# Optimization experiments

Measured on AMD Instinct MI355X. Metric: run time of the kernel, lower is better.

The kernel has to match this reference:

```python
import jax, jax.numpy as jnp
import numpy as np
from jax import lax

B, S, T = 32, 100, 4
NUM_C2, NUM_C3, NUM_D, DV = 500, 2000, 1000, 128


def setup_inputs():
    key = jax.random.key(0)
    ks = jax.random.split(key, 25)
    s = 0.05
    def nrm(k, shape):
        return jax.random.normal(k, shape, dtype=jnp.float32) * s
    return {
        "c2_seq": jax.random.randint(ks[0], (B, S), 0, NUM_C2),
        "c3_seq": jax.random.randint(ks[1], (B, S, T), 1, NUM_C3 + 1),  # 0 is padding; use all-valid tags
        "d_seq": jax.random.randint(ks[2], (B, S), 0, NUM_D),
        "r_seq": jax.random.randint(ks[3], (B, S), 0, 2),
        "D_emb": nrm(ks[4], (NUM_D, 1)),
        "R_emb": nrm(ks[5], (2, DV)),
        "v_c2": nrm(ks[6], (DV,)),
        "v_c3": nrm(ks[7], (DV,)),
        "v_d": nrm(ks[8], (DV,)),
        "W_ih": nrm(ks[9], (3 * DV, 2 * DV)),
        "W_hh": nrm(ks[10], (3 * DV, DV)),
        "b_ih": nrm(ks[11], (3 * DV,)),
        "b_hh": nrm(ks[12], (3 * DV,)),
        "l1_W1": nrm(ks[13], (DV, DV)), "l1_b1": nrm(ks[14], (DV,)),
        "l1_W2": nrm(ks[15], (1, DV)), "l1_b2": nrm(ks[16], (1,)),
        "l2_W1": nrm(ks[17], (DV, 4 * DV)), "l2_b1": nrm(ks[18], (DV,)),
        "l2_W2": nrm(ks[19], (1, DV)), "l2_b2": nrm(ks[20], (1,)),
        "l3_W1": nrm(ks[21], (DV, 4 * DV)), "l3_b1": nrm(ks[22], (DV,)),
        "l3_W2": nrm(ks[23], (1, DV)), "l3_b2": nrm(ks[24], (1,)),
    }


def _mlp(x, W1, b1, W2, b2):
    # Linear -> ReLU -> (Dropout: identity in eval) -> Linear -> (Dropout)
    return jnp.maximum(x @ W1.T + b1, 0.0) @ W2.T + b2


def _gru(x_seq, h0, W_ih, W_hh, b_ih, b_hh):
    # torch.nn.GRU math, batch_first
    def step(h, x):
        gi = x @ W_ih.T + b_ih
        gh = h @ W_hh.T + b_hh
        i_r, i_z, i_n = jnp.split(gi, 3, axis=-1)
        h_r, h_z, h_n = jnp.split(gh, 3, axis=-1)
        r = jax.nn.sigmoid(i_r + h_r)
        z = jax.nn.sigmoid(i_z + h_z)
        n = jnp.tanh(i_n + r * h_n)
        h_new = (1.0 - z) * n + z * h
        return h_new, h_new
    _, hs = lax.scan(step, h0, jnp.swapaxes(x_seq, 0, 1))
    return jnp.swapaxes(hs, 0, 1)


def _forward(c2_seq, c3_seq, d_seq, r_seq, p):
    (D_emb, R_emb, v_c2, v_c3, v_d, W_ih, W_hh, b_ih, b_hh,
     l1_W1, l1_b1, l1_W2, l1_b2, l2_W1, l2_b1, l2_W2, l2_b2,
     l3_W1, l3_b1, l3_W2, l3_b2) = p
    Bn = c2_seq.shape[0]
    gamma = D_emb[d_seq]                      # [B,S,1]
    v_d_seq = gamma * v_d                     # [B,S,DV]
    v_r_seq = R_emb[r_seq]                    # [B,S,DV]
    h0 = jnp.zeros((Bn, DV), dtype=v_d_seq.dtype)
    h_seq = _gru(jnp.concatenate([v_d_seq, v_r_seq], -1), h0, W_ih, W_hh, b_ih, b_hh)
    alpha_seq = _mlp(h_seq, l1_W1, l1_b1, l1_W2, l1_b2)[..., 0]   # [B,S]

    def step(carry, xs):
        C2, C3 = carry
        c2, c3, vd, vr = xs                                      # [B],[B,T],[B,DV],[B,DV]
        mask = (c3 != 0).astype(C3.dtype)                        # [B,T]
        w = mask / mask.sum(-1, keepdims=True)
        beta2 = jnp.take_along_axis(C2, c2[:, None], axis=-1)    # [B,1]
        beta3 = jnp.take_along_axis(C3, c3, axis=-1)             # [B,T]
        beta3_bar = (beta3 * w).sum(-1)                          # [B]
        vc2 = beta2 * v_c2                                       # [B,DV]
        vc3 = beta3[..., None] * v_c3                            # [B,T,DV]
        vc3_bar = beta3_bar[:, None] * v_c3                      # [B,DV]
        new_c2 = _mlp(jnp.concatenate([vc2, vc3_bar, vd, vr], -1),
                      l2_W1, l2_b1, l2_W2, l2_b2)[:, 0]          # [B]
        feat3 = jnp.concatenate([
            jnp.broadcast_to(vc2[:, None, :], vc3.shape), vc3,
            jnp.broadcast_to(vd[:, None, :], vc3.shape),
            jnp.broadcast_to(vr[:, None, :], vc3.shape)], -1)    # [B,T,4*DV]
        new_c3 = _mlp(feat3, l3_W1, l3_b1, l3_W2, l3_b2)[..., 0]  # [B,T]
        oh2 = jax.nn.one_hot(c2, NUM_C2, dtype=C2.dtype)          # [B,NC2]
        oh3 = jax.nn.one_hot(c3, NUM_C3 + 1, dtype=C3.dtype) * mask[..., None]  # [B,T,NC3+1]
        multi = oh3.sum(1)
        C2n = C2 * (1.0 - oh2) + new_c2[:, None] * oh2
        C3n = C3 * (1.0 - multi) + (new_c3[..., None] * oh3).sum(1)
        return (C2n, C3n), (C2n, C3n)

    C2_0 = jnp.zeros((Bn, NUM_C2), dtype=jnp.float32)
    C3_0 = jnp.zeros((Bn, NUM_C3 + 1), dtype=jnp.float32)
    xs = (jnp.swapaxes(c2_seq, 0, 1), jnp.swapaxes(c3_seq, 0, 1),
          jnp.swapaxes(v_d_seq, 0, 1), jnp.swapaxes(v_r_seq, 0, 1))
    _, (C2_seq, C3_seq) = lax.scan(step, (C2_0, C3_0), xs)
    C2_seq = jnp.swapaxes(C2_seq, 0, 1)   # [B,S,NUM_C2]
    C3_seq = jnp.swapaxes(C3_seq, 0, 1)   # [B,S,NUM_C3+1]
    return alpha_seq, h_seq, C2_seq, C3_seq


def reference(c2_seq, c3_seq, d_seq, r_seq, D_emb, R_emb, v_c2, v_c3, v_d,
              W_ih, W_hh, b_ih, b_hh, l1_W1, l1_b1, l1_W2, l1_b2,
              l2_W1, l2_b1, l2_W2, l2_b2, l3_W1, l3_b1, l3_W2, l3_b2):
    p = (D_emb, R_emb, v_c2, v_c3, v_d, W_ih, W_hh, b_ih, b_hh,
         l1_W1, l1_b1, l1_W2, l1_b2, l2_W1, l2_b1, l2_W2, l2_b2,
         l3_W1, l3_b1, l3_W2, l3_b2)
    return _forward(c2_seq, c3_seq, d_seq, r_seq, p)
```

## Files before the change

### kernel.cpp

```cpp
#include <hip/hip_runtime.h>

#define BB   32
#define SS   100
#define TT   4
#define NCC2 500
#define NC3P 2001
#define DD   128

#define LDSF 14680

typedef _Float16 half2v __attribute__((ext_vector_type(2)));

#if defined(__has_builtin)
#if __has_builtin(__builtin_amdgcn_fdot2)
#define HAVE_FDOT2 1
#endif
#endif

__device__ __forceinline__ float fast_rcp(float x) { return __builtin_amdgcn_rcpf(x); }

__device__ __forceinline__ float dpp_sum64(float x) {
    x += __int_as_float(__builtin_amdgcn_update_dpp(0, __float_as_int(x), 0x111, 0xf, 0xf, true));
    x += __int_as_float(__builtin_amdgcn_update_dpp(0, __float_as_int(x), 0x112, 0xf, 0xf, true));
    x += __int_as_float(__builtin_amdgcn_update_dpp(0, __float_as_int(x), 0x114, 0xf, 0xf, true));
    x += __int_as_float(__builtin_amdgcn_update_dpp(0, __float_as_int(x), 0x118, 0xf, 0xf, true));
    x += __int_as_float(__builtin_amdgcn_update_dpp(0, __float_as_int(x), 0x142, 0xa, 0xf, true));
    x += __int_as_float(__builtin_amdgcn_update_dpp(0, __float_as_int(x), 0x143, 0xc, 0xf, true));
    return x;
}

__device__ __forceinline__ float dpp_sum16(float x) {
    x += __int_as_float(__builtin_amdgcn_update_dpp(0, __float_as_int(x), 0x111, 0xf, 0xf, true));
    x += __int_as_float(__builtin_amdgcn_update_dpp(0, __float_as_int(x), 0x112, 0xf, 0xf, true));
    x += __int_as_float(__builtin_amdgcn_update_dpp(0, __float_as_int(x), 0x114, 0xf, 0xf, true));
    x += __int_as_float(__builtin_amdgcn_update_dpp(0, __float_as_int(x), 0x118, 0xf, 0xf, true));
    return x;
}

__device__ __forceinline__ float dot4(float4 a, float4 b) {
    return fmaf(a.x, b.x, fmaf(a.y, b.y, fmaf(a.z, b.z, a.w * b.w)));
}

__device__ __forceinline__ unsigned pk16(float a, float b) {
    return __builtin_bit_cast(unsigned, __builtin_amdgcn_cvt_pkrtz(a, b));
}
__device__ __forceinline__ uint4 packf16(float4 A, float4 B) {
    uint4 u;
    u.x = pk16(A.x, A.y); u.y = pk16(A.z, A.w);
    u.z = pk16(B.x, B.y); u.w = pk16(B.z, B.w);
    return u;
}

__device__ __forceinline__ float dot2acc(unsigned w, unsigned h, float acc) {
#ifdef HAVE_FDOT2
    return __builtin_amdgcn_fdot2(__builtin_bit_cast(half2v, w),
                                  __builtin_bit_cast(half2v, h), acc, false);
#else
    half2v a = __builtin_bit_cast(half2v, w), b = __builtin_bit_cast(half2v, h);
    acc = fmaf((float)a.x, (float)b.x, acc);
    return fmaf((float)a.y, (float)b.y, acc);
#endif
}

__global__ __launch_bounds__(768, 1) void k_main(
    const int* __restrict__ c2_seq, const int* __restrict__ c3_seq,
    const int* __restrict__ d_seq,  const int* __restrict__ r_seq,
    const float* __restrict__ D_emb, const float* __restrict__ Remb,
    const float* __restrict__ v_c2, const float* __restrict__ v_c3,
    const float* __restrict__ v_d,
    const float* __restrict__ W_ih, const float* __restrict__ W_hh,
    const float* __restrict__ b_ih, const float* __restrict__ b_hh,
    const float* __restrict__ l2W1, const float* __restrict__ l2b1,
    const float* __restrict__ l2W2, const float* __restrict__ l2b2,
    const float* __restrict__ l3W1, const float* __restrict__ l3b1,
    const float* __restrict__ l3W2, const float* __restrict__ l3b2,
    float* __restrict__ h_out, float* __restrict__ C2o, float* __restrict__ C3o)
{
    __shared__ __align__(16) float sh[LDSF];
    int* shi = (int*)sh;
    const int blk = blockIdx.x;
    const int t = threadIdx.x;

    if (blk < BB) {
        const int b  = blk;
        const int w  = t >> 6, l = t & 63;
        const int p4 = w & 3;
        const int j2 = (w >> 2) * 64 + l;
        const int jA = j2, jB = j2 + 192;
        const int kb = p4 * 32;

        uint4 wa0, wa1, wa2, wa3, wb0, wb1, wb2, wb3;
        {
            const float4* ra = (const float4*)(W_hh + jA * DD + kb);
            const float4* rb = (const float4*)(W_hh + jB * DD + kb);
            wa0 = packf16(ra[0], ra[1]); wa1 = packf16(ra[2], ra[3]);
            wa2 = packf16(ra[4], ra[5]); wa3 = packf16(ra[6], ra[7]);
            wb0 = packf16(rb[0], rb[1]); wb1 = packf16(rb[2], rb[3]);
            wb2 = packf16(rb[4], rb[5]); wb3 = packf16(rb[6], rb[7]);
        }

        {
            const float4* vd4 = (const float4*)(v_d + kb);
            const float4* r04 = (const float4*)(Remb + kb);
            const float4* r14 = (const float4*)(Remb + 128 + kb);
#pragma unroll
            for (int rr2 = 0; rr2 < 2; ++rr2) {
                const int j = rr2 ? jB : jA;
                const float4* wx = (const float4*)(W_ih + j * 256 + kb);
                const float4* wr = (const float4*)(W_ih + j * 256 + 128 + kb);
                float pd = 0.f, pr0 = 0.f, pr1 = 0.f;
#pragma unroll
                for (int i = 0; i < 8; ++i) {
                    float4 a = wx[i], c = wr[i];
                    float4 vd = vd4[i], r0 = r04[i], r1 = r14[i];
                    pd  = fmaf(a.x, vd.x, fmaf(a.y, vd.y, fmaf(a.z, vd.z, fmaf(a.w, vd.w, pd))));
                    pr0 = fmaf(c.x, r0.x, fmaf(c.y, r0.y, fmaf(c.z, r0.z, fmaf(c.w, r0.w, pr0))));
                    pr1 = fmaf(c.x, r1.x, fmaf(c.y, r1.y, fmaf(c.z, r1.z, fmaf(c.w, r1.w, pr1))));
                }
                sh[1880 + p4 * 388 + j] = pd;
                sh[3432 + p4 * 388 + j] = pr0;
                sh[4984 + p4 * 388 + j] = pr1;
            }
        }
        if (t < SS) {
            sh[1680 + t]  = D_emb[d_seq[b * SS + t]];
            shi[1780 + t] = r_seq[b * SS + t];
        }
        if (t < 64) ((unsigned*)sh)[t] = 0u;
        __syncthreads();

        float gd_r=0,gd_z=0,gd_n=0, g0_r=0,g0_z=0,g0_n=0, g1_r=0,g1_z=0,g1_n=0;
        float bi_r=0,bi_z=0,bi_n=0, bh_r=0,bh_z=0,bh_n=0, h = 0.f;
        if (t < DD) {
#pragma unroll
            for (int p = 0; p < 4; ++p) {
                gd_r += sh[1880 + p * 388 + t];
                gd_z += sh[1880 + p * 388 + 128 + t];
                gd_n += sh[1880 + p * 388 + 256 + t];
                g0_r += sh[3432 + p * 388 + t];
                g0_z += sh[3432 + p * 388 + 128 + t];
                g0_n += sh[3432 + p * 388 + 256 + t];
                g1_r += sh[4984 + p * 388 + t];
                g1_z += sh[4984 + p * 388 + 128 + t];
                g1_n += sh[4984 + p * 388 + 256 + t];
            }
            bi_r = b_ih[t]; bi_z = b_ih[t+128]; bi_n = b_ih[t+256];
            bh_r = b_hh[t]; bh_z = b_hh[t+128]; bh_n = b_hh[t+256];
        }
        __syncthreads();

        for (int s = 0; s < SS; ++s) {
            float aA = 0.f, aB = 0.f;
            {
                const uint4* hb = ((const uint4*)sh) + p4 * 4;
                uint4 h0 = hb[0], h1 = hb[1], h2 = hb[2], h3 = hb[3];
                aA = dot2acc(wa0.x, h0.x, aA); aA = dot2acc(wa0.y, h0.y, aA);
                aA = dot2acc(wa0.z, h0.z, aA); aA = dot2acc(wa0.w, h0.w, aA);
                aA = dot2acc(wa1.x, h1.x, aA); aA = dot2acc(wa1.y, h1.y, aA);
                aA = dot2acc(wa1.z, h1.z, aA); aA = dot2acc(wa1.w, h1.w, aA);
                aA = dot2acc(wa2.x, h2.x, aA); aA = dot2acc(wa2.y, h2.y, aA);
                aA = dot2acc(wa2.z, h2.z, aA); aA = dot2acc(wa2.w, h2.w, aA);
                aA = dot2acc(wa3.x, h3.x, aA); aA = dot2acc(wa3.y, h3.y, aA);
                aA = dot2acc(wa3.z, h3.z, aA); aA = dot2acc(wa3.w, h3.w, aA);
                aB = dot2acc(wb0.x, h0.x, aB); aB = dot2acc(wb0.y, h0.y, aB);
                aB = dot2acc(wb0.z, h0.z, aB); aB = dot2acc(wb0.w, h0.w, aB);
                aB = dot2acc(wb1.x, h1.x, aB); aB = dot2acc(wb1.y, h1.y, aB);
                aB = dot2acc(wb1.z, h1.z, aB); aB = dot2acc(wb1.w, h1.w, aB);
                aB = dot2acc(wb2.x, h2.x, aB); aB = dot2acc(wb2.y, h2.y, aB);
                aB = dot2acc(wb2.z, h2.z, aB); aB = dot2acc(wb2.w, h2.w, aB);
                aB = dot2acc(wb3.x, h3.x, aB); aB = dot2acc(wb3.y, h3.y, aB);
                aB = dot2acc(wb3.z, h3.z, aB); aB = dot2acc(wb3.w, h3.w, aB);
            }
            sh[128 + p4 * 388 + jA] = aA;
            sh[128 + p4 * 388 + jB] = aB;
            __syncthreads();
            if (t < DD) {
                float ghr = bh_r, ghz = bh_z, ghn = bh_n;
#pragma unroll
                for (int p = 0; p < 4; ++p) {
                    ghr += sh[128 + p * 388 + t];
                    ghz += sh[128 + p * 388 + 128 + t];
                    ghn += sh[128 + p * 388 + 256 + t];
                }
                float gamma = sh[1680 + s]; int rr = shi[1780 + s];
                float gir = fmaf(gamma, gd_r, (rr ? g1_r : g0_r) + bi_r);
                float giz = fmaf(gamma, gd_z, (rr ? g1_z : g0_z) + bi_z);
                float gin = fmaf(gamma, gd_n, (rr ? g1_n : g0_n) + bi_n);
                float r = fast_rcp(1.f + __expf(-(gir + ghr)));
                float z = fast_rcp(1.f + __expf(-(giz + ghz)));
                float n = 1.f - 2.f * fast_rcp(__expf(2.f * fmaf(r, ghn, gin)) + 1.f);
                h = (1.f - z) * n + z * h;
                ((_Float16*)sh)[t] = (_Float16)h;
                sh[1880 + s * DD + t] = h;
            }
            __syncthreads();
        }

        {
            const float4* hs = (const float4*)(sh + 1880);
            float4* hd = (float4*)(h_out + (size_t)b * SS * DD);
            for (int i = t; i < SS * DD / 4; i += 768) hd[i] = hs[i];
        }
    } else {
        const int sb = blk - BB;
        const int b = sb >> 2;
        const int q = sb & 3;

        {
            const int g = (t & 63) >> 4, c8 = ((t & 63) & 15) * 8;
            const float* vsrc = (g == 0) ? v_c2 : (g == 1) ? v_c3 : (g == 2) ? v_d : Remb;
            const float4 va  = *(const float4*)(vsrc + c8);
            const float4 vb  = *(const float4*)(vsrc + c8 + 4);
            const float4 va1 = *(const float4*)(Remb + 128 + c8);
            const float4 vb1 = *(const float4*)(Remb + 132 + c8);
            for (int r = t >> 6; r < 256; r += 12) {
                const float* W = (r < 128) ? l2W1 : l3W1;
                float* U = sh + ((r < 128) ? 3264 : 3904);
                const int i = r & 127;
                const float* wr = W + i * 512 + g * 128 + c8;
                const float4 w0 = *(const float4*)(wr);
                const float4 w1 = *(const float4*)(wr + 4);
                float p  = dot4(w0, va)  + dot4(w1, vb);
                float p1 = dot4(w0, va1) + dot4(w1, vb1);
                p  = dpp_sum16(p);
                p1 = dpp_sum16(p1);
                if ((t & 15) == 15) {
                    U[g * 128 + i] = p;
                    if (g == 3) U[512 + i] = p1;
                }
            }
        }
        for (int k = t; k < NCC2 + NC3P; k += 768) sh[k] = 0.f;
        for (int k = t; k < SS; k += 768) {
            shi[2504 + k] = c2_seq[b * SS + k];
            sh[3004 + k]  = D_emb[d_seq[b * SS + k]];
            shi[3104 + k] = r_seq[b * SS + k];
        }
        for (int k = t; k < SS; k += 768)
            reinterpret_cast<int4*>(shi + 2604)[k] = reinterpret_cast<const int4*>(c3_seq + b * SS * TT)[k];
        __syncthreads();

        if (t < 64) {
            float* C2s = sh;
            float* C3s = sh + NCC2;
            const float* u2 = sh + 3264;
            const float* u3 = sh + 3904;
            const float u2a0 = u2[t],        u2a1 = u2[64 + t];
            const float u2b0 = u2[128 + t],  u2b1 = u2[192 + t];
            const float u2c0 = u2[256 + t],  u2c1 = u2[320 + t];
            const float u2d00 = u2[384 + t], u2d01 = u2[448 + t];
            const float u2d10 = u2[512 + t], u2d11 = u2[576 + t];
            const float u3a0 = u3[t],        u3a1 = u3[64 + t];
            const float u3b0 = u3[128 + t],  u3b1 = u3[192 + t];
            const float u3c0 = u3[256 + t],  u3c1 = u3[320 + t];
            const float u3d00 = u3[384 + t], u3d01 = u3[448 + t];
            const float u3d10 = u3[512 + t], u3d11 = u3[576 + t];
            const float b2_0 = l2b1[t], b2_1 = l2b1[64 + t];
            const float w2_0 = l2W2[t], w2_1 = l2W2[64 + t];
            const float b3_0 = l3b1[t], b3_1 = l3b1[64 + t];
            const float w3_0 = l3W2[t], w3_1 = l3W2[64 + t];
            const float c2bias = l2b2[0], c3bias = l3b2[0];

            int  nc2 = shi[2504];
            int4 nc3 = reinterpret_cast<const int4*>(shi + 2604)[0];
            float ngam = sh[3004];
            int   nrr  = shi[3104];

            for (int s = 0; s < SS; ++s) {
                const int c2i = nc2;
                const int i0 = nc3.x, i1 = nc3.y, i2 = nc3.z, i3 = nc3.w;
                const float gamma = ngam;
                const int rr = nrr;
                if (s + 1 < SS) {
                    nc2 = shi[2504 + s + 1];
                    nc3 = reinterpret_cast<const int4*>(shi + 2604)[s + 1];
                    ngam = sh[3004 + s + 1];
                    nrr  = shi[3104 + s + 1];
                }

                const float beta2 = C2s[c2i];
                const bool k0 = (i0 != 0), k1 = (i1 != 0), k2 = (i2 != 0), k3 = (i3 != 0);
                const float m0 = k0 ? 1.f : 0.f, m1 = k1 ? 1.f : 0.f;
                const float m2 = k2 ? 1.f : 0.f, m3 = k3 ? 1.f : 0.f;
                const float bt0 = C3s[i0], bt1 = C3s[i1], bt2 = C3s[i2], bt3 = C3s[i3];
                const float msum = m0 + m1 + m2 + m3;
                const float b3bar = (bt0 * m0 + bt1 * m1 + bt2 * m2 + bt3 * m3) * fast_rcp(msum);

                const float ud20 = rr ? u2d10 : u2d00, ud21 = rr ? u2d11 : u2d01;
                const float ud30 = rr ? u3d10 : u3d00, ud31 = rr ? u3d11 : u3d01;

                float h20 = fmaf(beta2, u2a0, fmaf(b3bar, u2b0, fmaf(gamma, u2c0, ud20 + b2_0)));
                float h21 = fmaf(beta2, u2a1, fmaf(b3bar, u2b1, fmaf(gamma, u2c1, ud21 + b2_1)));
                float newc2 = dpp_sum64(fmaf(fmaxf(h20, 0.f), w2_0, fmaxf(h21, 0.f) * w2_1)) + c2bias;

                const float base30 = fmaf(beta2, u3a0, fmaf(gamma, u3c0, ud30 + b3_0));
                const float base31 = fmaf(beta2, u3a1, fmaf(gamma, u3c1, ud31 + b3_1));
                float ha, hb, q0, q1, q2, q3;
                ha = fmaf(bt0, u3b0, base30); hb = fmaf(bt0, u3b1, base31);
                q0 = dpp_sum64(fmaf(fmaxf(ha, 0.f), w3_0, fmaxf(hb, 0.f) * w3_1)) + c3bias;
                ha = fmaf(bt1, u3b0, base30); hb = fmaf(bt1, u3b1, base31);
                q1 = dpp_sum64(fmaf(fmaxf(ha, 0.f), w3_0, fmaxf(hb, 0.f) * w3_1)) + c3bias;
                ha = fmaf(bt2, u3b0, base30); hb = fmaf(bt2, u3b1, base31);
                q2 = dpp_sum64(fmaf(fmaxf(ha, 0.f), w3_0, fmaxf(hb, 0.f) * w3_1)) + c3bias;
                ha = fmaf(bt3, u3b0, base30); hb = fmaf(bt3, u3b1, base31);
                q3 = dpp_sum64(fmaf(fmaxf(ha, 0.f), w3_0, fmaxf(hb, 0.f) * w3_1)) + c3bias;

                float val0, val1, val2, val3;
                {
                    float c = m0 + ((k1 && i1 == i0) ? 1.f : 0.f) + ((k2 && i2 == i0) ? 1.f : 0.f) + ((k3 && i3 == i0) ? 1.f : 0.f);
                    float qs = (k0 ? q0 : 0.f) + ((k1 && i1 == i0) ? q1 : 0.f) + ((k2 && i2 == i0) ? q2 : 0.f) + ((k3 && i3 == i0) ? q3 : 0.f);
                    val0 = bt0 * (1.f - c) + qs;
                }
                {
                    float c = ((k0 && i0 == i1) ? 1.f : 0.f) + m1 + ((k2 && i2 == i1) ? 1.f : 0.f) + ((k3 && i3 == i1) ? 1.f : 0.f);
                    float qs = ((k0 && i0 == i1) ? q0 : 0.f) + (k1 ? q1 : 0.f) + ((k2 && i2 == i1) ? q2 : 0.f) + ((k3 && i3 == i1) ? q3 : 0.f);
                    val1 = bt1 * (1.f - c) + qs;
                }
                {
                    float c = ((k0 && i0 == i2) ? 1.f : 0.f) + ((k1 && i1 == i2) ? 1.f : 0.f) + m2 + ((k3 && i3 == i2) ? 1.f : 0.f);
                    float qs = ((k0 && i0 == i2) ? q0 : 0.f) + ((k1 && i1 == i2) ? q1 : 0.f) + (k2 ? q2 : 0.f) + ((k3 && i3 == i2) ? q3 : 0.f);
                    val2 = bt2 * (1.f - c) + qs;
                }
                {
                    float c = ((k0 && i0 == i3) ? 1.f : 0.f) + ((k1 && i1 == i3) ? 1.f : 0.f) + ((k2 && i2 == i3) ? 1.f : 0.f) + m3;
                    float qs = ((k0 && i0 == i3) ? q0 : 0.f) + ((k1 && i1 == i3) ? q1 : 0.f) + ((k2 && i2 == i3) ? q2 : 0.f) + (k3 ? q3 : 0.f);
                    val3 = bt3 * (1.f - c) + qs;
                }

                if (t == 63) {
                    C2s[c2i] = newc2;
                    if (k0) C3s[i0] = val0;
                    if (k1) C3s[i1] = val1;
                    if (k2) C3s[i2] = val2;
                    if (k3) C3s[i3] = val3;
                    sh[4544 + s] = newc2;
                    sh[4644 + 4 * s + 0] = val0;
                    sh[4644 + 4 * s + 1] = val1;
                    sh[4644 + 4 * s + 2] = val2;
                    sh[4644 + 4 * s + 3] = val3;
                }
            }
        }
        __syncthreads();

        for (int k = t; k < NCC2 + NC3P; k += 768) sh[k] = 0.f;
        __syncthreads();

        float* C2s = sh;
        float* C3s = sh + NCC2;
        for (int s = 0; s < SS; ++s) {
            if (t == 0) {
                C2s[shi[2504 + s]] = sh[4544 + s];
                const int4 ic3 = reinterpret_cast<const int4*>(shi + 2604)[s];
                if (ic3.x) C3s[ic3.x] = sh[4644 + 4 * s + 0];
                if (ic3.y) C3s[ic3.y] = sh[4644 + 4 * s + 1];
                if (ic3.z) C3s[ic3.z] = sh[4644 + 4 * s + 2];
                if (ic3.w) C3s[ic3.w] = sh[4644 + 4 * s + 3];
            }
            if ((s & 3) == q) {
                __syncthreads();
                const int rs = b * SS + s;
                float* c2row = C2o + (size_t)rs * NCC2;
                if (t < 125) reinterpret_cast<float4*>(c2row)[t] = reinterpret_cast<const float4*>(C2s)[t];
                float* c3row = C3o + (size_t)rs * NC3P;
                const int p0 = (4 - (rs & 3)) & 3;
                if (t < p0) c3row[t] = C3s[t];
                const int rem = NC3P - p0;
                const int nv = rem >> 2, tl = rem & 3;
                if (t < nv) {
                    const int d = p0 + 4 * t;
                    *reinterpret_cast<float4*>(c3row + d) =
                        make_float4(C3s[d], C3s[d + 1], C3s[d + 2], C3s[d + 3]);
                }
                if (t < tl) {
                    const int d = p0 + 4 * nv + t;
                    c3row[d] = C3s[d];
                }
                __syncthreads();
            }
        }
    }
}

__global__ __launch_bounds__(256) void k_alpha(const float* __restrict__ h_seq,
                                               const float* __restrict__ W1,
                                               const float* __restrict__ b1,
                                               const float* __restrict__ W2,
                                               const float* __restrict__ b2,
                                               float* __restrict__ alpha)
{
    __shared__ __align__(16) float sl[22560];
    const int t = threadIdx.x;
    const int base = blockIdx.x * 16;

    float4* hl4 = reinterpret_cast<float4*>(sl);
    const float4* hg = reinterpret_cast<const float4*>(h_seq + (size_t)base * DD);
    for (int i = t; i < 512; i += 256) hl4[i] = hg[i];

    float4* wl4 = reinterpret_cast<float4*>(sl + 6144);
    const float4* wg = reinterpret_cast<const float4*>(W1);
    for (int g = t; g < 4096; g += 256) {
        const int ch = g >> 5, k4 = g & 31;
        wl4[ch * 32 + (k4 ^ (ch & 31))] = wg[g];
    }
    __syncthreads();

    const int ch = t & 127, half = t >> 7;
    float acc[16];
#pragma unroll
    for (int r = 0; r < 16; ++r) acc[r] = 0.f;
#pragma unroll
    for (int kk = 0; kk < 16; ++kk) {
        const int k4 = half * 16 + kk;
        const float4 w = wl4[ch * 32 + (k4 ^ (ch & 31))];
#pragma unroll
        for (int r = 0; r < 16; ++r) {
            const float4 hv = hl4[r * 32 + k4];
            acc[r] = fmaf(w.x, hv.x, fmaf(w.y, hv.y, fmaf(w.z, hv.z, fmaf(w.w, hv.w, acc[r]))));
        }
    }
#pragma unroll
    for (int r = 0; r < 16; ++r) sl[2048 + r * 256 + t] = acc[r];
    __syncthreads();
    if (t < 128) {
        const float b1v = b1[t], w2v = W2[t];
#pragma unroll
        for (int r = 0; r < 16; ++r) {
            float v = fmaxf(sl[2048 + r * 256 + t] + sl[2048 + r * 256 + 128 + t] + b1v, 0.f) * w2v;
            v = dpp_sum64(v);
            if ((t & 63) == 63) sl[22528 + r * 2 + (t >> 6)] = v;
        }
    }
    __syncthreads();
    if (t < 16) alpha[base + t] = sl[22528 + 2 * t] + sl[22528 + 2 * t + 1] + b2[0];
}

extern "C" void kernel_launch(void* const* d_in, const int* in_sizes, int n_in,
                              void* d_out, int out_size, void* d_ws, size_t ws_size,
                              hipStream_t stream)
{
    (void)in_sizes; (void)n_in; (void)out_size; (void)d_ws; (void)ws_size;
    const int*   c2_seq = (const int*)d_in[0];
    const int*   c3_seq = (const int*)d_in[1];
    const int*   d_seq  = (const int*)d_in[2];
    const int*   r_seq  = (const int*)d_in[3];
    const float* D_emb  = (const float*)d_in[4];
    const float* Remb   = (const float*)d_in[5];
    const float* v_c2   = (const float*)d_in[6];
    const float* v_c3   = (const float*)d_in[7];
    const float* v_d    = (const float*)d_in[8];
    const float* W_ih   = (const float*)d_in[9];
    const float* W_hh   = (const float*)d_in[10];
    const float* b_ih   = (const float*)d_in[11];
    const float* b_hh   = (const float*)d_in[12];
    const float* l1W1   = (const float*)d_in[13];
    const float* l1b1   = (const float*)d_in[14];
    const float* l1W2   = (const float*)d_in[15];
    const float* l1b2   = (const float*)d_in[16];
    const float* l2W1   = (const float*)d_in[17];
    const float* l2b1   = (const float*)d_in[18];
    const float* l2W2   = (const float*)d_in[19];
    const float* l2b2   = (const float*)d_in[20];
    const float* l3W1   = (const float*)d_in[21];
    const float* l3b1   = (const float*)d_in[22];
    const float* l3W2   = (const float*)d_in[23];
    const float* l3b2   = (const float*)d_in[24];

    float* out   = (float*)d_out;
    float* alpha = out;
    float* h_out = out + 3200;
    float* C2o   = out + 412800;
    float* C3o   = out + 2012800;

    k_main<<<BB + 4 * BB, 768, 0, stream>>>(c2_seq, c3_seq, d_seq, r_seq, D_emb, Remb,
                                            v_c2, v_c3, v_d,
                                            W_ih, W_hh, b_ih, b_hh,
                                            l2W1, l2b1, l2W2, l2b2,
                                            l3W1, l3b1, l3W2, l3b2,
                                            h_out, C2o, C3o);
    k_alpha<<<200, 256, 0, stream>>>(h_out, l1W1, l1b1, l1W2, l1b2, alpha);
}
```

Baseline: 118.4 us.

## Split fused GRU/scan kernel into separate kernels and widen scan output split

```diff
diff --git a/kernel.cpp b/kernel.cpp
--- a/kernel.cpp
+++ b/kernel.cpp
@@ -6,8 +6,6 @@
 #define NCC2 500
 #define NC3P 2001
 #define DD   128
-
-#define LDSF 14680
 
 typedef _Float16 half2v __attribute__((ext_vector_type(2)));
 
@@ -62,322 +60,328 @@
 #endif
 }
 
-__global__ __launch_bounds__(768, 1) void k_main(
+__global__ __launch_bounds__(768, 1) void k_gru(
+    const int* __restrict__ d_seq,  const int* __restrict__ r_seq,
+    const float* __restrict__ D_emb, const float* __restrict__ Remb,
+    const float* __restrict__ v_d,
+    const float* __restrict__ W_ih, const float* __restrict__ W_hh,
+    const float* __restrict__ b_ih, const float* __restrict__ b_hh,
+    float* __restrict__ h_out)
+{
+    __shared__ __align__(16) float sh[14680];
+    int* shi = (int*)sh;
+    const int b = blockIdx.x;
+    const int t = threadIdx.x;
+
+    const int w  = t >> 6, l = t & 63;
+    const int p4 = w & 3;
+    const int j2 = (w >> 2) * 64 + l;
+    const int jA = j2, jB = j2 + 192;
+    const int kb = p4 * 32;
+
+    uint4 wa0, wa1, wa2, wa3, wb0, wb1, wb2, wb3;
+    {
+        const float4* ra = (const float4*)(W_hh + jA * DD + kb);
+        const float4* rb = (const float4*)(W_hh + jB * DD + kb);
+        wa0 = packf16(ra[0], ra[1]); wa1 = packf16(ra[2], ra[3]);
+        wa2 = packf16(ra[4], ra[5]); wa3 = packf16(ra[6], ra[7]);
+        wb0 = packf16(rb[0], rb[1]); wb1 = packf16(rb[2], rb[3]);
+        wb2 = packf16(rb[4], rb[5]); wb3 = packf16(rb[6], rb[7]);
+    }
+
+    {
+        const float4* vd4 = (const float4*)(v_d + kb);
+        const float4* r04 = (const float4*)(Remb + kb);
+        const float4* r14 = (const float4*)(Remb + 128 + kb);
+#pragma unroll
+        for (int rr2 = 0; rr2 < 2; ++rr2) {
+            const int j = rr2 ? jB : jA;
+            const float4* wx = (const float4*)(W_ih + j * 256 + kb);
+            const float4* wr = (const float4*)(W_ih + j * 256 + 128 + kb);
+            float pd = 0.f, pr0 = 0.f, pr1 = 0.f;
+#pragma unroll
+            for (int i = 0; i < 8; ++i) {
+                float4 a = wx[i], c = wr[i];
+                float4 vd = vd4[i], r0 = r04[i], r1 = r14[i];
+                pd  = fmaf(a.x, vd.x, fmaf(a.y, vd.y, fmaf(a.z, vd.z, fmaf(a.w, vd.w, pd))));
+                pr0 = fmaf(c.x, r0.x, fmaf(c.y, r0.y, fmaf(c.z, r0.z, fmaf(c.w, r0.w, pr0))));
+                pr1 = fmaf(c.x, r1.x, fmaf(c.y, r1.y, fmaf(c.z, r1.z, fmaf(c.w, r1.w, pr1))));
+            }
+            sh[1880 + p4 * 388 + j] = pd;
+            sh[3432 + p4 * 388 + j] = pr0;
+            sh[4984 + p4 * 388 + j] = pr1;
+        }
+    }
+    if (t < SS) {
+        sh[1680 + t]  = D_emb[d_seq[b * SS + t]];
+        shi[1780 + t] = r_seq[b * SS + t];
+    }
+    if (t < 64) ((unsigned*)sh)[t] = 0u;
+    __syncthreads();
+
+    float gd_r=0,gd_z=0,gd_n=0, g0_r=0,g0_z=0,g0_n=0, g1_r=0,g1_z=0,g1_n=0;
+    float bi_r=0,bi_z=0,bi_n=0, bh_r=0,bh_z=0,bh_n=0, h = 0.f;
+    if (t < DD) {
+#pragma unroll
+        for (int p = 0; p < 4; ++p) {
+            gd_r += sh[1880 + p * 388 + t];
+            gd_z += sh[1880 + p * 388 + 128 + t];
+            gd_n += sh[1880 + p * 388 + 256 + t];
+            g0_r += sh[3432 + p * 388 + t];
+            g0_z += sh[3432 + p * 388 + 128 + t];
+            g0_n += sh[3432 + p * 388 + 256 + t];
+            g1_r += sh[4984 + p * 388 + t];
+            g1_z += sh[4984 + p * 388 + 128 + t];
+            g1_n += sh[4984 + p * 388 + 256 + t];
+        }
+        bi_r = b_ih[t]; bi_z = b_ih[t+128]; bi_n = b_ih[t+256];
+        bh_r = b_hh[t]; bh_z = b_hh[t+128]; bh_n = b_hh[t+256];
+    }
+    __syncthreads();
+
+    for (int s = 0; s < SS; ++s) {
+        float aA = 0.f, aB = 0.f;
+        {
+            const uint4* hb = ((const uint4*)sh) + p4 * 4;
+            uint4 h0 = hb[0], h1 = hb[1], h2 = hb[2], h3 = hb[3];
+            aA = dot2acc(wa0.x, h0.x, aA); aA = dot2acc(wa0.y, h0.y, aA);
+            aA = dot2acc(wa0.z, h0.z, aA); aA = dot2acc(wa0.w, h0.w, aA);
+            aA = dot2acc(wa1.x, h1.x, aA); aA = dot2acc(wa1.y, h1.y, aA);
+            aA = dot2acc(wa1.z, h1.z, aA); aA = dot2acc(wa1.w, h1.w, aA);
+            aA = dot2acc(wa2.x, h2.x, aA); aA = dot2acc(wa2.y, h2.y, aA);
+            aA = dot2acc(wa2.z, h2.z, aA); aA = dot2acc(wa2.w, h2.w, aA);
+            aA = dot2acc(wa3.x, h3.x, aA); aA = dot2acc(wa3.y, h3.y, aA);
+            aA = dot2acc(wa3.z, h3.z, aA); aA = dot2acc(wa3.w, h3.w, aA);
+            aB = dot2acc(wb0.x, h0.x, aB); aB = dot2acc(wb0.y, h0.y, aB);
+            aB = dot2acc(wb0.z, h0.z, aB); aB = dot2acc(wb0.w, h0.w, aB);
+            aB = dot2acc(wb1.x, h1.x, aB); aB = dot2acc(wb1.y, h1.y, aB);
+            aB = dot2acc(wb1.z, h1.z, aB); aB = dot2acc(wb1.w, h1.w, aB);
+            aB = dot2acc(wb2.x, h2.x, aB); aB = dot2acc(wb2.y, h2.y, aB);
+            aB = dot2acc(wb2.z, h2.z, aB); aB = dot2acc(wb2.w, h2.w, aB);
+            aB = dot2acc(wb3.x, h3.x, aB); aB = dot2acc(wb3.y, h3.y, aB);
+            aB = dot2acc(wb3.z, h3.z, aB); aB = dot2acc(wb3.w, h3.w, aB);
+        }
+        sh[128 + p4 * 388 + jA] = aA;
+        sh[128 + p4 * 388 + jB] = aB;
+        __syncthreads();
+        if (t < DD) {
+            float ghr = bh_r, ghz = bh_z, ghn = bh_n;
+#pragma unroll
+            for (int p = 0; p < 4; ++p) {
+                ghr += sh[128 + p * 388 + t];
+                ghz += sh[128 + p * 388 + 128 + t];
+                ghn += sh[128 + p * 388 + 256 + t];
+            }
+            float gamma = sh[1680 + s]; int rr = shi[1780 + s];
+            float gir = fmaf(gamma, gd_r, (rr ? g1_r : g0_r) + bi_r);
+            float giz = fmaf(gamma, gd_z, (rr ? g1_z : g0_z) + bi_z);
+            float gin = fmaf(gamma, gd_n, (rr ? g1_n : g0_n) + bi_n);
+            float r = fast_rcp(1.f + __expf(-(gir + ghr)));
+            float z = fast_rcp(1.f + __expf(-(giz + ghz)));
+            float n = 1.f - 2.f * fast_rcp(__expf(2.f * fmaf(r, ghn, gin)) + 1.f);
+            h = (1.f - z) * n + z * h;
+            ((_Float16*)sh)[t] = (_Float16)h;
+            sh[1880 + s * DD + t] = h;
+        }
+        __syncthreads();
+    }
+
+    {
+        const float4* hs = (const float4*)(sh + 1880);
+        float4* hd = (float4*)(h_out + (size_t)b * SS * DD);
+        for (int i = t; i < SS * DD / 4; i += 768) hd[i] = hs[i];
+    }
+}
+
+__global__ __launch_bounds__(512, 1) void k_scan(
     const int* __restrict__ c2_seq, const int* __restrict__ c3_seq,
     const int* __restrict__ d_seq,  const int* __restrict__ r_seq,
     const float* __restrict__ D_emb, const float* __restrict__ Remb,
     const float* __restrict__ v_c2, const float* __restrict__ v_c3,
     const float* __restrict__ v_d,
-    const float* __restrict__ W_ih, const float* __restrict__ W_hh,
-    const float* __restrict__ b_ih, const float* __restrict__ b_hh,
     const float* __restrict__ l2W1, const float* __restrict__ l2b1,
     const float* __restrict__ l2W2, const float* __restrict__ l2b2,
     const float* __restrict__ l3W1, const float* __restrict__ l3b1,
     const float* __restrict__ l3W2, const float* __restrict__ l3b2,
-    float* __restrict__ h_out, float* __restrict__ C2o, float* __restrict__ C3o)
+    float* __restrict__ C2o, float* __restrict__ C3o)
 {
-    __shared__ __align__(16) float sh[LDSF];
+    __shared__ __align__(16) float sh[5044];
     int* shi = (int*)sh;
-    const int blk = blockIdx.x;
     const int t = threadIdx.x;
-
-    if (blk < BB) {
-        const int b  = blk;
-        const int w  = t >> 6, l = t & 63;
-        const int p4 = w & 3;
-        const int j2 = (w >> 2) * 64 + l;
-        const int jA = j2, jB = j2 + 192;
-        const int kb = p4 * 32;
-
-        uint4 wa0, wa1, wa2, wa3, wb0, wb1, wb2, wb3;
-        {
-            const float4* ra = (const float4*)(W_hh + jA * DD + kb);
-            const float4* rb = (const float4*)(W_hh + jB * DD + kb);
-            wa0 = packf16(ra[0], ra[1]); wa1 = packf16(ra[2], ra[3]);
-            wa2 = packf16(ra[4], ra[5]); wa3 = packf16(ra[6], ra[7]);
-            wb0 = packf16(rb[0], rb[1]); wb1 = packf16(rb[2], rb[3]);
-            wb2 = packf16(rb[4], rb[5]); wb3 = packf16(rb[6], rb[7]);
-        }
-
-        {
-            const float4* vd4 = (const float4*)(v_d + kb);
-            const float4* r04 = (const float4*)(Remb + kb);
-            const float4* r14 = (const float4*)(Remb + 128 + kb);
-#pragma unroll
-            for (int rr2 = 0; rr2 < 2; ++rr2) {
-                const int j = rr2 ? jB : jA;
-                const float4* wx = (const float4*)(W_ih + j * 256 + kb);
-                const float4* wr = (const float4*)(W_ih + j * 256 + 128 + kb);
-                float pd = 0.f, pr0 = 0.f, pr1 = 0.f;
-#pragma unroll
-                for (int i = 0; i < 8; ++i) {
-                    float4 a = wx[i], c = wr[i];
-                    float4 vd = vd4[i], r0 = r04[i], r1 = r14[i];
-                    pd  = fmaf(a.x, vd.x, fmaf(a.y, vd.y, fmaf(a.z, vd.z, fmaf(a.w, vd.w, pd))));
-                    pr0 = fmaf(c.x, r0.x, fmaf(c.y, r0.y, fmaf(c.z, r0.z, fmaf(c.w, r0.w, pr0))));
-                    pr1 = fmaf(c.x, r1.x, fmaf(c.y, r1.y, fmaf(c.z, r1.z, fmaf(c.w, r1.w, pr1))));
-                }
-                sh[1880 + p4 * 388 + j] = pd;
-                sh[3432 + p4 * 388 + j] = pr0;
-                sh[4984 + p4 * 388 + j] = pr1;
-            }
-        }
-        if (t < SS) {
-            sh[1680 + t]  = D_emb[d_seq[b * SS + t]];
-            shi[1780 + t] = r_seq[b * SS + t];
-        }
-        if (t < 64) ((unsigned*)sh)[t] = 0u;
-        __syncthreads();
-
-        float gd_r=0,gd_z=0,gd_n=0, g0_r=0,g0_z=0,g0_n=0, g1_r=0,g1_z=0,g1_n=0;
-        float bi_r=0,bi_z=0,bi_n=0, bh_r=0,bh_z=0,bh_n=0, h = 0.f;
-        if (t < DD) {
-#pragma unroll
-            for (int p = 0; p < 4; ++p) {
-                gd_r += sh[1880 + p * 388 + t];
-                gd_z += sh[1880 + p * 388 + 128 + t];
-                gd_n += sh[1880 + p * 388 + 256 + t];
-                g0_r += sh[3432 + p * 388 + t];
-                g0_z += sh[3432 + p * 388 + 128 + t];
-                g0_n += sh[3432 + p * 388 + 256 + t];
-                g1_r += sh[4984 + p * 388 + t];
-                g1_z += sh[4984 + p * 388 + 128 + t];
-                g1_n += sh[4984 + p * 388 + 256 + t];
-            }
-            bi_r = b_ih[t]; bi_z = b_ih[t+128]; bi_n = b_ih[t+256];
-            bh_r = b_hh[t]; bh_z = b_hh[t+128]; bh_n = b_hh[t+256];
-        }
-        __syncthreads();
-
-        for (int s = 0; s < SS; ++s) {
-            float aA = 0.f, aB = 0.f;
-            {
-                const uint4* hb = ((const uint4*)sh) + p4 * 4;
-                uint4 h0 = hb[0], h1 = hb[1], h2 = hb[2], h3 = hb[3];
-                aA = dot2acc(wa0.x, h0.x, aA); aA = dot2acc(wa0.y, h0.y, aA);
-                aA = dot2acc(wa0.z, h0.z, aA); aA = dot2acc(wa0.w, h0.w, aA);
-                aA = dot2acc(wa1.x, h1.x, aA); aA = dot2acc(wa1.y, h1.y, aA);
-                aA = dot2acc(wa1.z, h1.z, aA); aA = dot2acc(wa1.w, h1.w, aA);
-                aA = dot2acc(wa2.x, h2.x, aA); aA = dot2acc(wa2.y, h2.y, aA);
-                aA = dot2acc(wa2.z, h2.z, aA); aA = dot2acc(wa2.w, h2.w, aA);
-                aA = dot2acc(wa3.x, h3.x, aA); aA = dot2acc(wa3.y, h3.y, aA);
-                aA = dot2acc(wa3.z, h3.z, aA); aA = dot2acc(wa3.w, h3.w, aA);
-                aB = dot2acc(wb0.x, h0.x, aB); aB = dot2acc(wb0.y, h0.y, aB);
-                aB = dot2acc(wb0.z, h0.z, aB); aB = dot2acc(wb0.w, h0.w, aB);
-                aB = dot2acc(wb1.x, h1.x, aB); aB = dot2acc(wb1.y, h1.y, aB);
-                aB = dot2acc(wb1.z, h1.z, aB); aB = dot2acc(wb1.w, h1.w, aB);
-                aB = dot2acc(wb2.x, h2.x, aB); aB = dot2acc(wb2.y, h2.y, aB);
-                aB = dot2acc(wb2.z, h2.z, aB); aB = dot2acc(wb2.w, h2.w, aB);
-                aB = dot2acc(wb3.x, h3.x, aB); aB = dot2acc(wb3.y, h3.y, aB);
-                aB = dot2acc(wb3.z, h3.z, aB); aB = dot2acc(wb3.w, h3.w, aB);
-            }
-            sh[128 + p4 * 388 + jA] = aA;
-            sh[128 + p4 * 388 + jB] = aB;
-            __syncthreads();
-            if (t < DD) {
-                float ghr = bh_r, ghz = bh_z, ghn = bh_n;
-#pragma unroll
-                for (int p = 0; p < 4; ++p) {
-                    ghr += sh[128 + p * 388 + t];
-                    ghz += sh[128 + p * 388 + 128 + t];
-                    ghn += sh[128 + p * 388 + 256 + t];
-                }
-                float gamma = sh[1680 + s]; int rr = shi[1780 + s];
-                float gir = fmaf(gamma, gd_r, (rr ? g1_r : g0_r) + bi_r);
-                float giz = fmaf(gamma, gd_z, (rr ? g1_z : g0_z) + bi_z);
-                float gin = fmaf(gamma, gd_n, (rr ? g1_n : g0_n) + bi_n);
-                float r = fast_rcp(1.f + __expf(-(gir + ghr)));
-                float z = fast_rcp(1.f + __expf(-(giz + ghz)));
-                float n = 1.f - 2.f * fast_rcp(__expf(2.f * fmaf(r, ghn, gin)) + 1.f);
-                h = (1.f - z) * n + z * h;
-                ((_Float16*)sh)[t] = (_Float16)h;
-                sh[1880 + s * DD + t] = h;
-            }
-            __syncthreads();
-        }
-
-        {
-            const float4* hs = (const float4*)(sh + 1880);
-            float4* hd = (float4*)(h_out + (size_t)b * SS * DD);
-            for (int i = t; i < SS * DD / 4; i += 768) hd[i] = hs[i];
-        }
-    } else {
-        const int sb = blk - BB;
-        const int b = sb >> 2;
-        const int q = sb & 3;
-
-        {
-            const int g = (t & 63) >> 4, c8 = ((t & 63) & 15) * 8;
-            const float* vsrc = (g == 0) ? v_c2 : (g == 1) ? v_c3 : (g == 2) ? v_d : Remb;
-            const float4 va  = *(const float4*)(vsrc + c8);
-            const float4 vb  = *(const float4*)(vsrc + c8 + 4);
-            const float4 va1 = *(const float4*)(Remb + 128 + c8);
-            const float4 vb1 = *(const float4*)(Remb + 132 + c8);
-            for (int r = t >> 6; r < 256; r += 12) {
-                const float* W = (r < 128) ? l2W1 : l3W1;
-                float* U = sh + ((r < 128) ? 3264 : 3904);
-                const int i = r & 127;
-                const float* wr = W + i * 512 + g * 128 + c8;
-                const float4 w0 = *(const float4*)(wr);
-                const float4 w1 = *(const float4*)(wr + 4);
-                float p  = dot4(w0, va)  + dot4(w1, vb);
-                float p1 = dot4(w0, va1) + dot4(w1, vb1);
-                p  = dpp_sum16(p);
-                p1 = dpp_sum16(p1);
-                if ((t & 15) == 15) {
-                    U[g * 128 + i] = p;
-                    if (g == 3) U[512 + i] = p1;
-                }
-            }
-        }
-        for (int k = t; k < NCC2 + NC3P; k += 768) sh[k] = 0.f;
-        for (int k = t; k < SS; k += 768) {
-            shi[2504 + k] = c2_seq[b * SS + k];
-            sh[3004 + k]  = D_emb[d_seq[b * SS + k]];
-            shi[3104 + k] = r_seq[b * SS + k];
-        }
-        for (int k = t; k < SS; k += 768)
-            reinterpret_cast<int4*>(shi + 2604)[k] = reinterpret_cast<const int4*>(c3_seq + b * SS * TT)[k];
-        __syncthreads();
-
-        if (t < 64) {
-            float* C2s = sh;
-            float* C3s = sh + NCC2;
-            const float* u2 = sh + 3264;
-            const float* u3 = sh + 3904;
-            const float u2a0 = u2[t],        u2a1 = u2[64 + t];
-            const float u2b0 = u2[128 + t],  u2b1 = u2[192 + t];
-            const float u2c0 = u2[256 + t],  u2c1 = u2[320 + t];
-            const float u2d00 = u2[384 + t], u2d01 = u2[448 + t];
-            const float u2d10 = u2[512 + t], u2d11 = u2[576 + t];
-            const float u3a0 = u3[t],        u3a1 = u3[64 + t];
-            const float u3b0 = u3[128 + t],  u3b1 = u3[192 + t];
-            const float u3c0 = u3[256 + t],  u3c1 = u3[320 + t];
-            const float u3d00 = u3[384 + t], u3d01 = u3[448 + t];
-            const float u3d10 = u3[512 + t], u3d11 = u3[576 + t];
-            const float b2_0 = l2b1[t], b2_1 = l2b1[64 + t];
-            const float w2_0 = l2W2[t], w2_1 = l2W2[64 + t];
-            const float b3_0 = l3b1[t], b3_1 = l3b1[64 + t];
-            const float w3_0 = l3W2[t], w3_1 = l3W2[64 + t];
-            const float c2bias = l2b2[0], c3bias = l3b2[0];
-
-            int  nc2 = shi[2504];
-            int4 nc3 = reinterpret_cast<const int4*>(shi + 2604)[0];
-            float ngam = sh[3004];
-            int   nrr  = shi[3104];
-
-            for (int s = 0; s < SS; ++s) {
-                const int c2i = nc2;
-                const int i0 = nc3.x, i1 = nc3.y, i2 = nc3.z, i3 = nc3.w;
-                const float gamma = ngam;
-                const int rr = nrr;
-                if (s + 1 < SS) {
-                    nc2 = shi[2504 + s + 1];
-                    nc3 = reinterpret_cast<const int4*>(shi + 2604)[s + 1];
-                    ngam = sh[3004 + s + 1];
-                    nrr  = shi[3104 + s + 1];
-                }
-
-                const float beta2 = C2s[c2i];
-                const bool k0 = (i0 != 0), k1 = (i1 != 0), k2 = (i2 != 0), k3 = (i3 != 0);
-                const float m0 = k0 ? 1.f : 0.f, m1 = k1 ? 1.f : 0.f;
-                const float m2 = k2 ? 1.f : 0.f, m3 = k3 ? 1.f : 0.f;
-                const float bt0 = C3s[i0], bt1 = C3s[i1], bt2 = C3s[i2], bt3 = C3s[i3];
-                const float msum = m0 + m1 + m2 + m3;
-                const float b3bar = (bt0 * m0 + bt1 * m1 + bt2 * m2 + bt3 * m3) * fast_rcp(msum);
-
-                const float ud20 = rr ? u2d10 : u2d00, ud21 = rr ? u2d11 : u2d01;
-                const float ud30 = rr ? u3d10 : u3d00, ud31 = rr ? u3d11 : u3d01;
-
-                float h20 = fmaf(beta2, u2a0, fmaf(b3bar, u2b0, fmaf(gamma, u2c0, ud20 + b2_0)));
-                float h21 = fmaf(beta2, u2a1, fmaf(b3bar, u2b1, fmaf(gamma, u2c1, ud21 + b2_1)));
-                float newc2 = dpp_sum64(fmaf(fmaxf(h20, 0.f), w2_0, fmaxf(h21, 0.f) * w2_1)) + c2bias;
-
-                const float base30 = fmaf(beta2, u3a0, fmaf(gamma, u3c0, ud30 + b3_0));
-                const float base31 = fmaf(beta2, u3a1, fmaf(gamma, u3c1, ud31 + b3_1));
-                float ha, hb, q0, q1, q2, q3;
-                ha = fmaf(bt0, u3b0, base30); hb = fmaf(bt0, u3b1, base31);
-                q0 = dpp_sum64(fmaf(fmaxf(ha, 0.f), w3_0, fmaxf(hb, 0.f) * w3_1)) + c3bias;
-                ha = fmaf(bt1, u3b0, base30); hb = fmaf(bt1, u3b1, base31);
-                q1 = dpp_sum64(fmaf(fmaxf(ha, 0.f), w3_0, fmaxf(hb, 0.f) * w3_1)) + c3bias;
-                ha = fmaf(bt2, u3b0, base30); hb = fmaf(bt2, u3b1, base31);
-                q2 = dpp_sum64(fmaf(fmaxf(ha, 0.f), w3_0, fmaxf(hb, 0.f) * w3_1)) + c3bias;
-                ha = fmaf(bt3, u3b0, base30); hb = fmaf(bt3, u3b1, base31);
-                q3 = dpp_sum64(fmaf(fmaxf(ha, 0.f), w3_0, fmaxf(hb, 0.f) * w3_1)) + c3bias;
-
-                float val0, val1, val2, val3;
-                {
-                    float c = m0 + ((k1 && i1 == i0) ? 1.f : 0.f) + ((k2 && i2 == i0) ? 1.f : 0.f) + ((k3 && i3 == i0) ? 1.f : 0.f);
-                    float qs = (k0 ? q0 : 0.f) + ((k1 && i1 == i0) ? q1 : 0.f) + ((k2 && i2 == i0) ? q2 : 0.f) + ((k3 && i3 == i0) ? q3 : 0.f);
-                    val0 = bt0 * (1.f - c) + qs;
-                }
-                {
-                    float c = ((k0 && i0 == i1) ? 1.f : 0.f) + m1 + ((k2 && i2 == i1) ? 1.f : 0.f) + ((k3 && i3 == i1) ? 1.f : 0.f);
-                    float qs = ((k0 && i0 == i1) ? q0 : 0.f) + (k1 ? q1 : 0.f) + ((k2 && i2 == i1) ? q2 : 0.f) + ((k3 && i3 == i1) ? q3 : 0.f);
-                    val1 = bt1 * (1.f - c) + qs;
-                }
-                {
-                    float c = ((k0 && i0 == i2) ? 1.f : 0.f) + ((k1 && i1 == i2) ? 1.f : 0.f) + m2 + ((k3 && i3 == i2) ? 1.f : 0.f);
-                    float qs = ((k0 && i0 == i2) ? q0 : 0.f) + ((k1 && i1 == i2) ? q1 : 0.f) + (k2 ? q2 : 0.f) + ((k3 && i3 == i2) ? q3 : 0.f);
-                    val2 = bt2 * (1.f - c) + qs;
-                }
-                {
-                    float c = ((k0 && i0 == i3) ? 1.f : 0.f) + ((k1 && i1 == i3) ? 1.f : 0.f) + ((k2 && i2 == i3) ? 1.f : 0.f) + m3;
-                    float qs = ((k0 && i0 == i3) ? q0 : 0.f) + ((k1 && i1 == i3) ? q1 : 0.f) + ((k2 && i2 == i3) ? q2 : 0.f) + (k3 ? q3 : 0.f);
-                    val3 = bt3 * (1.f - c) + qs;
-                }
-
-                if (t == 63) {
-                    C2s[c2i] = newc2;
-                    if (k0) C3s[i0] = val0;
-                    if (k1) C3s[i1] = val1;
-                    if (k2) C3s[i2] = val2;
-                    if (k3) C3s[i3] = val3;
-                    sh[4544 + s] = newc2;
-                    sh[4644 + 4 * s + 0] = val0;
-                    sh[4644 + 4 * s + 1] = val1;
-                    sh[4644 + 4 * s + 2] = val2;
-                    sh[4644 + 4 * s + 3] = val3;
-                }
-            }
-        }
-        __syncthreads();
-
-        for (int k = t; k < NCC2 + NC3P; k += 768) sh[k] = 0.f;
-        __syncthreads();
-
+    const int b = blockIdx.x >> 3;
+    const int q = blockIdx.x & 7;
+
+    {
+        const int g = (t & 63) >> 4, c8 = ((t & 63) & 15) * 8;
+        const float* vsrc = (g == 0) ? v_c2 : (g == 1) ? v_c3 : (g == 2) ? v_d : Remb;
+        const float4 va  = *(const float4*)(vsrc + c8);
+        const float4 vb  = *(const float4*)(vsrc + c8 + 4);
+        const float4 va1 = *(const float4*)(Remb + 128 + c8);
+        const float4 vb1 = *(const float4*)(Remb + 132 + c8);
+        for (int r = t >> 6; r < 256; r += 8) {
+            const float* W = (r < 128) ? l2W1 : l3W1;
+            float* U = sh + ((r < 128) ? 3264 : 3904);
+            const int i = r & 127;
+            const float* wr = W + i * 512 + g * 128 + c8;
+            const float4 w0 = *(const float4*)(wr);
+            const float4 w1 = *(const float4*)(wr + 4);
+            float p  = dot4(w0, va)  + dot4(w1, vb);
+            float p1 = dot4(w0, va1) + dot4(w1, vb1);
+            p  = dpp_sum16(p);
+            p1 = dpp_sum16(p1);
+            if ((t & 15) == 15) {
+                U[g * 128 + i] = p;
+                if (g == 3) U[512 + i] = p1;
+            }
+        }
+    }
+    for (int k = t; k < NCC2 + NC3P; k += 512) sh[k] = 0.f;
+    for (int k = t; k < SS; k += 512) {
+        shi[2504 + k] = c2_seq[b * SS + k];
+        sh[3004 + k]  = D_emb[d_seq[b * SS + k]];
+        shi[3104 + k] = r_seq[b * SS + k];
+    }
+    for (int k = t; k < SS; k += 512)
+        reinterpret_cast<int4*>(shi + 2604)[k] = reinterpret_cast<const int4*>(c3_seq + b * SS * TT)[k];
+    __syncthreads();
+
+    if (t < 64) {
         float* C2s = sh;
         float* C3s = sh + NCC2;
+        const float* u2 = sh + 3264;
+        const float* u3 = sh + 3904;
+        const float u2a0 = u2[t],        u2a1 = u2[64 + t];
+        const float u2b0 = u2[128 + t],  u2b1 = u2[192 + t];
+        const float u2c0 = u2[256 + t],  u2c1 = u2[320 + t];
+        const float u2d00 = u2[384 + t], u2d01 = u2[448 + t];
+        const float u2d10 = u2[512 + t], u2d11 = u2[576 + t];
+        const float u3a0 = u3[t],        u3a1 = u3[64 + t];
+        const float u3b0 = u3[128 + t],  u3b1 = u3[192 + t];
+        const float u3c0 = u3[256 + t],  u3c1 = u3[320 + t];
+        const float u3d00 = u3[384 + t], u3d01 = u3[448 + t];
+        const float u3d10 = u3[512 + t], u3d11 = u3[576 + t];
+        const float b2_0 = l2b1[t], b2_1 = l2b1[64 + t];
+        const float w2_0 = l2W2[t], w2_1 = l2W2[64 + t];
+        const float b3_0 = l3b1[t], b3_1 = l3b1[64 + t];
+        const float w3_0 = l3W2[t], w3_1 = l3W2[64 + t];
+        const float c2bias = l2b2[0], c3bias = l3b2[0];
+
+        int  nc2 = shi[2504];
+        int4 nc3 = reinterpret_cast<const int4*>(shi + 2604)[0];
+        float ngam = sh[3004];
+        int   nrr  = shi[3104];
+
         for (int s = 0; s < SS; ++s) {
-            if (t == 0) {
-                C2s[shi[2504 + s]] = sh[4544 + s];
-                const int4 ic3 = reinterpret_cast<const int4*>(shi + 2604)[s];
-                if (ic3.x) C3s[ic3.x] = sh[4644 + 4 * s + 0];
-                if (ic3.y) C3s[ic3.y] = sh[4644 + 4 * s + 1];
-                if (ic3.z) C3s[ic3.z] = sh[4644 + 4 * s + 2];
-                if (ic3.w) C3s[ic3.w] = sh[4644 + 4 * s + 3];
-            }
-            if ((s & 3) == q) {
-                __syncthreads();
-                const int rs = b * SS + s;
-                float* c2row = C2o + (size_t)rs * NCC2;
-                if (t < 125) reinterpret_cast<float4*>(c2row)[t] = reinterpret_cast<const float4*>(C2s)[t];
-                float* c3row = C3o + (size_t)rs * NC3P;
-                const int p0 = (4 - (rs & 3)) & 3;
-                if (t < p0) c3row[t] = C3s[t];
-                const int rem = NC3P - p0;
-                const int nv = rem >> 2, tl = rem & 3;
-                if (t < nv) {
-                    const int d = p0 + 4 * t;
-                    *reinterpret_cast<float4*>(c3row + d) =
-                        make_float4(C3s[d], C3s[d + 1], C3s[d + 2], C3s[d + 3]);
-                }
-                if (t < tl) {
-                    const int d = p0 + 4 * nv + t;
-                    c3row[d] = C3s[d];
-                }
-                __syncthreads();
-            }
+            const int c2i = nc2;
+            const int i0 = nc3.x, i1 = nc3.y, i2 = nc3.z, i3 = nc3.w;
+            const float gamma = ngam;
+            const int rr = nrr;
+            if (s + 1 < SS) {
+                nc2 = shi[2504 + s + 1];
+                nc3 = reinterpret_cast<const int4*>(shi + 2604)[s + 1];
+                ngam = sh[3004 + s + 1];
+                nrr  = shi[3104 + s + 1];
+            }
+
+            const float beta2 = C2s[c2i];
+            const bool k0 = (i0 != 0), k1 = (i1 != 0), k2 = (i2 != 0), k3 = (i3 != 0);
+            const float m0 = k0 ? 1.f : 0.f, m1 = k1 ? 1.f : 0.f;
+            const float m2 = k2 ? 1.f : 0.f, m3 = k3 ? 1.f : 0.f;
+            const float bt0 = C3s[i0], bt1 = C3s[i1], bt2 = C3s[i2], bt3 = C3s[i3];
+            const float msum = m0 + m1 + m2 + m3;
+            const float b3bar = (bt0 * m0 + bt1 * m1 + bt2 * m2 + bt3 * m3) * fast_rcp(msum);
+
+            const float ud20 = rr ? u2d10 : u2d00, ud21 = rr ? u2d11 : u2d01;
+            const float ud30 = rr ? u3d10 : u3d00, ud31 = rr ? u3d11 : u3d01;
+
+            float h20 = fmaf(beta2, u2a0, fmaf(b3bar, u2b0, fmaf(gamma, u2c0, ud20 + b2_0)));
+            float h21 = fmaf(beta2, u2a1, fmaf(b3bar, u2b1, fmaf(gamma, u2c1, ud21 + b2_1)));
+            float newc2 = dpp_sum64(fmaf(fmaxf(h20, 0.f), w2_0, fmaxf(h21, 0.f) * w2_1)) + c2bias;
+
+            const float base30 = fmaf(beta2, u3a0, fmaf(gamma, u3c0, ud30 + b3_0));
+            const float base31 = fmaf(beta2, u3a1, fmaf(gamma, u3c1, ud31 + b3_1));
+            float ha, hb, q0, q1, q2, q3;
+            ha = fmaf(bt0, u3b0, base30); hb = fmaf(bt0, u3b1, base31);
+            q0 = dpp_sum64(fmaf(fmaxf(ha, 0.f), w3_0, fmaxf(hb, 0.f) * w3_1)) + c3bias;
+            ha = fmaf(bt1, u3b0, base30); hb = fmaf(bt1, u3b1, base31);
+            q1 = dpp_sum64(fmaf(fmaxf(ha, 0.f), w3_0, fmaxf(hb, 0.f) * w3_1)) + c3bias;
+            ha = fmaf(bt2, u3b0, base30); hb = fmaf(bt2, u3b1, base31);
+            q2 = dpp_sum64(fmaf(fmaxf(ha, 0.f), w3_0, fmaxf(hb, 0.f) * w3_1)) + c3bias;
+            ha = fmaf(bt3, u3b0, base30); hb = fmaf(bt3, u3b1, base31);
+            q3 = dpp_sum64(fmaf(fmaxf(ha, 0.f), w3_0, fmaxf(hb, 0.f) * w3_1)) + c3bias;
+
+            float val0, val1, val2, val3;
+            {
+                float c = m0 + ((k1 && i1 == i0) ? 1.f : 0.f) + ((k2 && i2 == i0) ? 1.f : 0.f) + ((k3 && i3 == i0) ? 1.f : 0.f);
+                float qs = (k0 ? q0 : 0.f) + ((k1 && i1 == i0) ? q1 : 0.f) + ((k2 && i2 == i0) ? q2 : 0.f) + ((k3 && i3 == i0) ? q3 : 0.f);
+                val0 = bt0 * (1.f - c) + qs;
+            }
+            {
+                float c = ((k0 && i0 == i1) ? 1.f : 0.f) + m1 + ((k2 && i2 == i1) ? 1.f : 0.f) + ((k3 && i3 == i1) ? 1.f : 0.f);
+                float qs = ((k0 && i0 == i1) ? q0 : 0.f) + (k1 ? q1 : 0.f) + ((k2 && i2 == i1) ? q2 : 0.f) + ((k3 && i3 == i1) ? q3 : 0.f);
+                val1 = bt1 * (1.f - c) + qs;
+            }
+            {
+                float c = ((k0 && i0 == i2) ? 1.f : 0.f) + ((k1 && i1 == i2) ? 1.f : 0.f) + m2 + ((k3 && i3 == i2) ? 1.f : 0.f);
+                float qs = ((k0 && i0 == i2) ? q0 : 0.f) + ((k1 && i1 == i2) ? q1 : 0.f) + (k2 ? q2 : 0.f) + ((k3 && i3 == i2) ? q3 : 0.f);
+                val2 = bt2 * (1.f - c) + qs;
+            }
+            {
+                float c = ((k0 && i0 == i3) ? 1.f : 0.f) + ((k1 && i1 == i3) ? 1.f : 0.f) + ((k2 && i2 == i3) ? 1.f : 0.f) + m3;
+                float qs = ((k0 && i0 == i3) ? q0 : 0.f) + ((k1 && i1 == i3) ? q1 : 0.f) + ((k2 && i2 == i3) ? q2 : 0.f) + (k3 ? q3 : 0.f);
+                val3 = bt3 * (1.f - c) + qs;
+            }
+
+            if (t == 63) {
+                C2s[c2i] = newc2;
+                if (k0) C3s[i0] = val0;
+                if (k1) C3s[i1] = val1;
+                if (k2) C3s[i2] = val2;
+                if (k3) C3s[i3] = val3;
+                sh[4544 + s] = newc2;
+                sh[4644 + 4 * s + 0] = val0;
+                sh[4644 + 4 * s + 1] = val1;
+                sh[4644 + 4 * s + 2] = val2;
+                sh[4644 + 4 * s + 3] = val3;
+            }
+        }
+    }
+    __syncthreads();
+
+    for (int k = t; k < NCC2 + NC3P; k += 512) sh[k] = 0.f;
+    __syncthreads();
+
+    float* C2s = sh;
+    float* C3s = sh + NCC2;
+    for (int s = 0; s < SS; ++s) {
+        if (t == 0) {
+            C2s[shi[2504 + s]] = sh[4544 + s];
+            const int4 ic3 = reinterpret_cast<const int4*>(shi + 2604)[s];
+            if (ic3.x) C3s[ic3.x] = sh[4644 + 4 * s + 0];
+            if (ic3.y) C3s[ic3.y] = sh[4644 + 4 * s + 1];
+            if (ic3.z) C3s[ic3.z] = sh[4644 + 4 * s + 2];
+            if (ic3.w) C3s[ic3.w] = sh[4644 + 4 * s + 3];
+        }
+        if ((s & 7) == q) {
+            __syncthreads();
+            const int rs = b * SS + s;
+            float* c2row = C2o + (size_t)rs * NCC2;
+            if (t < 125) reinterpret_cast<float4*>(c2row)[t] = reinterpret_cast<const float4*>(C2s)[t];
+            float* c3row = C3o + (size_t)rs * NC3P;
+            const int p0 = (4 - (rs & 3)) & 3;
+            if (t < p0) c3row[t] = C3s[t];
+            const int rem = NC3P - p0;
+            const int nv = rem >> 2, tl = rem & 3;
+            if (t < nv) {
+                const int d = p0 + 4 * t;
+                *reinterpret_cast<float4*>(c3row + d) =
+                    make_float4(C3s[d], C3s[d + 1], C3s[d + 2], C3s[d + 3]);
+            }
+            if (t < tl) {
+                const int d = p0 + 4 * nv + t;
+                c3row[d] = C3s[d];
+            }
+            __syncthreads();
         }
     }
 }
@@ -472,11 +476,12 @@
     float* C2o   = out + 412800;
     float* C3o   = out + 2012800;
 
-    k_main<<<BB + 4 * BB, 768, 0, stream>>>(c2_seq, c3_seq, d_seq, r_seq, D_emb, Remb,
-                                            v_c2, v_c3, v_d,
-                                            W_ih, W_hh, b_ih, b_hh,
-                                            l2W1, l2b1, l2W2, l2b2,
-                                            l3W1, l3b1, l3W2, l3b2,
-                                            h_out, C2o, C3o);
+    k_gru<<<BB, 768, 0, stream>>>(d_seq, r_seq, D_emb, Remb, v_d,
+                                  W_ih, W_hh, b_ih, b_hh, h_out);
+    k_scan<<<8 * BB, 512, 0, stream>>>(c2_seq, c3_seq, d_seq, r_seq, D_emb, Remb,
+                                       v_c2, v_c3, v_d,
+                                       l2W1, l2b1, l2W2, l2b2,
+                                       l3W1, l3b1, l3W2, l3b2,
+                                       C2o, C3o);
     k_alpha<<<200, 256, 0, stream>>>(h_out, l1W1, l1b1, l1W2, l1b2, alpha);
 }
```

Result: slower. 197.7 us (+67.0%).
